# Kernel tuning notes

Hardware: AMD Instinct MI355X
Metric: run time of the kernel (lower is better)

## Reference

```python
import jax, jax.numpy as jnp
import numpy as np

T, B, D_MODEL, H, FFN = 2048, 2, 128, 8, 1024
EPS = 1e-5
NEG = -1e9


def setup_inputs() -> dict:
    key = jax.random.key(0)
    ks = jax.random.split(key, 20)
    d = D_MODEL
    w = lambda k, sh: (jax.random.normal(k, sh, jnp.float32) * 0.02)
    z = lambda n: jnp.zeros((n,), jnp.float32)
    o = lambda n: jnp.ones((n,), jnp.float32)
    return {
        "x": jax.random.normal(ks[0], (T, B, d), jnp.float32),
        "enc": jax.random.normal(ks[1], (T, B, d), jnp.float32),
        "sa_wq": w(ks[2], (d, d)), "sa_bq": z(d),
        "sa_wk": w(ks[3], (d, d)), "sa_bk": z(d),
        "sa_wv": w(ks[4], (d, d)), "sa_bv": z(d),
        "sa_wo": w(ks[5], (d, d)), "sa_bo": z(d),
        "ln1_g": o(d), "ln1_b": z(d),
        "ca_wq": w(ks[6], (d, d)), "ca_bq": z(d),
        "ca_wk": w(ks[7], (d, d)), "ca_bk": z(d),
        "ca_wv": w(ks[8], (d, d)), "ca_bv": z(d),
        "ca_wo": w(ks[9], (d, d)), "ca_bo": z(d),
        "ln2_g": o(d), "ln2_b": z(d),
        "fc1_w": w(ks[10], (d, FFN)), "fc1_b": z(FFN),
        "fc2_w": w(ks[11], (FFN, d)), "fc2_b": z(d),
        "ln3_g": o(d), "ln3_b": z(d),
    }


def _ln(x, g, b):
    m = jnp.mean(x, -1, keepdims=True)
    v = jnp.mean(jnp.square(x - m), -1, keepdims=True)
    return (x - m) * jax.lax.rsqrt(v + EPS) * g + b


def _mha(q_in, kv_in, wq, bq, wk, bk, wv, bv, wo, bo, mask):
    # q_in: [T, B, C]; kv_in: [S, B, C]  (Time x Batch x Channel, as in torch src)
    Tq, Bz, C = q_in.shape
    S = kv_in.shape[0]
    Dh = C // H
    q = (q_in @ wq + bq) * (Dh ** -0.5)
    k = kv_in @ wk + bk
    v = kv_in @ wv + bv
    q = q.reshape(Tq, Bz, H, Dh)
    k = k.reshape(S, Bz, H, Dh)
    v = v.reshape(S, Bz, H, Dh)
    scores = jnp.einsum('tbhd,sbhd->bhts', q, k)  # materialized [B,H,T,S]
    if mask is not None:
        scores = scores + mask  # additive causal mask, broadcast over b,h
    probs = jax.nn.softmax(scores, axis=-1)
    out = jnp.einsum('bhts,sbhd->tbhd', probs, v).reshape(Tq, Bz, C)
    return out @ wo + bo


def reference(x, enc,
              sa_wq, sa_bq, sa_wk, sa_bk, sa_wv, sa_bv, sa_wo, sa_bo,
              ln1_g, ln1_b,
              ca_wq, ca_bq, ca_wk, ca_bk, ca_wv, ca_bv, ca_wo, ca_bo,
              ln2_g, ln2_b,
              fc1_w, fc1_b, fc2_w, fc2_b,
              ln3_g, ln3_b):
    Tq = x.shape[0]
    causal = jnp.where(jnp.tril(jnp.ones((Tq, Tq), bool)), 0.0, NEG).astype(x.dtype)
    # self-attention block (post-norm, dropout=0 in eval)
    res = x
    x = res + _mha(x, x, sa_wq, sa_bq, sa_wk, sa_bk, sa_wv, sa_bv, sa_wo, sa_bo, causal)
    x = _ln(x, ln1_g, ln1_b)
    # cross-attention block
    res = x
    x = res + _mha(x, enc, ca_wq, ca_bq, ca_wk, ca_bk, ca_wv, ca_bv, ca_wo, ca_bo, None)
    x = _ln(x, ln2_g, ln2_b)
    # FFN block (exact erf gelu, matching torch F.gelu default)
    res = x
    h = jax.nn.gelu(x @ fc1_w + fc1_b, approximate=False)
    x = res + (h @ fc2_w + fc2_b)
    x = _ln(x, ln3_g, ln3_b)
    return x
```

## Files before the change

kernel.cpp:

```cpp
#include <hip/hip_runtime.h>
#include <hip/hip_bf16.h>

#define TT 2048
#define BB 2
#define DM 128
#define HH 8
#define DH 16
#define FFN_N 1024
#define ROWS (TT * BB)
#define EPS_LN 1e-5f
#define NC 8
#define SC (TT / NC)
#define NQ32 (TT / 32)
#define NQP (TT / 64)
#define NBH (BB * HH)

typedef __attribute__((ext_vector_type(8))) short bf16x8;
typedef __attribute__((ext_vector_type(4))) short bf16x4v;
typedef __attribute__((ext_vector_type(4))) float f32x4;
typedef __attribute__((ext_vector_type(16))) float f32x16;

__device__ __forceinline__ short f2bf(float x) {
    __hip_bfloat16 h = __float2bfloat16(x);
    union { __hip_bfloat16 hh; short s; } u; u.hh = h; return u.s;
}

__global__ __launch_bounds__(256) void cvt2(
    const float* __restrict__ a, const float* __restrict__ b,
    short* __restrict__ oa, short* __restrict__ ob, int n)
{
    int i = (blockIdx.x * 256 + threadIdx.x) * 4;
    const float* src = a; short* dst = oa;
    if (i >= n) { i -= n; src = b; dst = ob; }
    float4 f = *(const float4*)(src + i);
    bf16x4v o;
    o[0] = f2bf(f.x); o[1] = f2bf(f.y); o[2] = f2bf(f.z); o[3] = f2bf(f.w);
    *(bf16x4v*)(dst + i) = o;
}

__global__ __launch_bounds__(256) void cvt_w_all(
    const float* w0, const float* w1, const float* w2, const float* w3,
    const float* w4, const float* w5, const float* w6, const float* w7,
    const float* w8, const float* w9,
    short* o0, short* o1, short* o2, short* o3,
    short* o4, short* o5, short* o6, short* o7,
    short* o8, short* o9)
{
    const float* srcs[10] = {w0, w1, w2, w3, w4, w5, w6, w7, w8, w9};
    short* dsts[10] = {o0, o1, o2, o3, o4, o5, o6, o7, o8, o9};
    const int bx = blockIdx.x;
    int wi, tile, K, N;
    if (bx < 128)      { wi = bx >> 4; tile = bx & 15;  K = 128;  N = 128;  }
    else if (bx < 256) { wi = 8;       tile = bx - 128; K = 128;  N = 1024; }
    else               { wi = 9;       tile = bx - 256; K = 1024; N = 128;  }
    const float* src = srcs[wi];
    short* dst = dsts[wi];
    const int ntx = N >> 5;
    const int k0 = (tile / ntx) << 5;
    const int n0 = (tile % ntx) << 5;

    __shared__ float sm[32][33];
    const int j = threadIdx.x & 31;
    const int i0 = threadIdx.x >> 5;
    #pragma unroll
    for (int p = 0; p < 4; ++p) {
        const int ii = i0 + p * 8;
        sm[ii][j] = src[(size_t)(k0 + ii) * N + n0 + j];
    }
    __syncthreads();
    #pragma unroll
    for (int p = 0; p < 4; ++p) {
        const int ii = i0 + p * 8;
        dst[(size_t)(n0 + ii) * K + k0 + j] = f2bf(sm[j][ii]);
    }
}

template<int MODE, int GELU>
__global__ __launch_bounds__(256) void gemm_mfma(
    const short* __restrict__ A, const short* __restrict__ Wt,
    const float* __restrict__ bias, void* __restrict__ outp,
    int M, int N, int K, float scale)
{
    const int tid = threadIdx.x;
    const int w = tid >> 6, lane = tid & 63;
    const int wm = w >> 1, wn = w & 1;
    const int g = lane >> 4, qi = lane & 15;
    const int bm = blockIdx.y * 64 + wm * 32;
    const int bn = blockIdx.x * 64 + wn * 32;

    f32x4 acc[2][2];
    #pragma unroll
    for (int a = 0; a < 2; ++a)
        #pragma unroll
        for (int b = 0; b < 2; ++b) acc[a][b] = (f32x4){0.f, 0.f, 0.f, 0.f};

    for (int k0 = 0; k0 < K; k0 += 32) {
        bf16x8 af[2], bf[2];
        #pragma unroll
        for (int fm = 0; fm < 2; ++fm) {
            const short* p = A + (size_t)(bm + fm * 16 + qi) * K + k0 + g * 4;
            bf16x4v lo = *(const bf16x4v*)p;
            bf16x4v hi = *(const bf16x4v*)(p + 16);
            af[fm][0] = lo[0]; af[fm][1] = lo[1]; af[fm][2] = lo[2]; af[fm][3] = lo[3];
            af[fm][4] = hi[0]; af[fm][5] = hi[1]; af[fm][6] = hi[2]; af[fm][7] = hi[3];
        }
        #pragma unroll
        for (int fn = 0; fn < 2; ++fn) {
            const short* p = Wt + (size_t)(bn + fn * 16 + qi) * K + k0 + g * 4;
            bf16x4v lo = *(const bf16x4v*)p;
            bf16x4v hi = *(const bf16x4v*)(p + 16);
            bf[fn][0] = lo[0]; bf[fn][1] = lo[1]; bf[fn][2] = lo[2]; bf[fn][3] = lo[3];
            bf[fn][4] = hi[0]; bf[fn][5] = hi[1]; bf[fn][6] = hi[2]; bf[fn][7] = hi[3];
        }
        #pragma unroll
        for (int fm = 0; fm < 2; ++fm)
            #pragma unroll
            for (int fn = 0; fn < 2; ++fn)
                acc[fm][fn] = __builtin_amdgcn_mfma_f32_16x16x32_bf16(
                    af[fm], bf[fn], acc[fm][fn], 0, 0, 0);
    }

    #pragma unroll
    for (int fm = 0; fm < 2; ++fm)
        #pragma unroll
        for (int fn = 0; fn < 2; ++fn)
            #pragma unroll
            for (int r = 0; r < 4; ++r) {
                const int m = bm + fm * 16 + g * 4 + r;
                const int n = bn + fn * 16 + qi;
                float v = (acc[fm][fn][r] + bias[n]) * scale;
                if (GELU) v = 0.5f * v * (1.f + erff(v * 0.70710678118654752f));
                ((short*)outp)[(size_t)m * N + n] = f2bf(v);
            }
}

__global__ __launch_bounds__(256) void qkv_gemm(
    const short* __restrict__ A0, const short* __restrict__ A1, const short* __restrict__ A2,
    const short* __restrict__ W0, const short* __restrict__ W1, const short* __restrict__ W2,
    const float* __restrict__ B0, const float* __restrict__ B1, const float* __restrict__ B2,
    short* __restrict__ O0, short* __restrict__ O1, short* __restrict__ O2,
    float s0)
{
    const int z = blockIdx.z;
    const short* A = (z == 0) ? A0 : (z == 1) ? A1 : A2;
    const short* Wt = (z == 0) ? W0 : (z == 1) ? W1 : W2;
    const float* bias = (z == 0) ? B0 : (z == 1) ? B1 : B2;
    short* out = (z == 0) ? O0 : (z == 1) ? O1 : O2;
    const float scale = (z == 0) ? s0 : 1.f;
    const int K = DM, N = DM;

    const int tid = threadIdx.x;
    const int w = tid >> 6, lane = tid & 63;
    const int wm = w >> 1, wn = w & 1;
    const int g = lane >> 4, qi = lane & 15;
    const int bm = blockIdx.y * 64 + wm * 32;
    const int bn = blockIdx.x * 64 + wn * 32;

    f32x4 acc[2][2];
    #pragma unroll
    for (int a = 0; a < 2; ++a)
        #pragma unroll
        for (int b = 0; b < 2; ++b) acc[a][b] = (f32x4){0.f, 0.f, 0.f, 0.f};

    for (int k0 = 0; k0 < K; k0 += 32) {
        bf16x8 af[2], bf[2];
        #pragma unroll
        for (int fm = 0; fm < 2; ++fm) {
            const short* p = A + (size_t)(bm + fm * 16 + qi) * K + k0 + g * 4;
            bf16x4v lo = *(const bf16x4v*)p;
            bf16x4v hi = *(const bf16x4v*)(p + 16);
            af[fm][0] = lo[0]; af[fm][1] = lo[1]; af[fm][2] = lo[2]; af[fm][3] = lo[3];
            af[fm][4] = hi[0]; af[fm][5] = hi[1]; af[fm][6] = hi[2]; af[fm][7] = hi[3];
        }
        #pragma unroll
        for (int fn = 0; fn < 2; ++fn) {
            const short* p = Wt + (size_t)(bn + fn * 16 + qi) * K + k0 + g * 4;
            bf16x4v lo = *(const bf16x4v*)p;
            bf16x4v hi = *(const bf16x4v*)(p + 16);
            bf[fn][0] = lo[0]; bf[fn][1] = lo[1]; bf[fn][2] = lo[2]; bf[fn][3] = lo[3];
            bf[fn][4] = hi[0]; bf[fn][5] = hi[1]; bf[fn][6] = hi[2]; bf[fn][7] = hi[3];
        }
        #pragma unroll
        for (int fm = 0; fm < 2; ++fm)
            #pragma unroll
            for (int fn = 0; fn < 2; ++fn)
                acc[fm][fn] = __builtin_amdgcn_mfma_f32_16x16x32_bf16(
                    af[fm], bf[fn], acc[fm][fn], 0, 0, 0);
    }

    #pragma unroll
    for (int fm = 0; fm < 2; ++fm)
        #pragma unroll
        for (int fn = 0; fn < 2; ++fn)
            #pragma unroll
            for (int r = 0; r < 4; ++r) {
                const int m = bm + fm * 16 + g * 4 + r;
                const int n = bn + fn * 16 + qi;
                const float v = (acc[fm][fn][r] + bias[n]) * scale;
                const int t = m >> 1, bz = m & 1, hH = n >> 4, d = n & 15;
                size_t idx;
                if (z < 2) {
                    const int dp = ((d >> 2) & 1) * 8 + (d & 3) + ((d >> 3) & 1) * 4;
                    idx = ((size_t)(bz * HH + hH) * TT + t) * DH + dp;
                } else {
                    const int u = t & 15;
                    const int tp = (t & ~15) | (((u >> 2) & 1) * 8 + (u & 3) + ((u >> 3) & 1) * 4);
                    idx = ((size_t)(bz * HH + hH) * DH + d) * TT + tp;
                }
                out[idx] = f2bf(v);
            }
}

template<int CAUSAL>
__global__ __launch_bounds__(256, 4) void attn_part(
    const short* __restrict__ Qh, const short* __restrict__ Kh,
    const short* __restrict__ Vt, float* __restrict__ pacc,
    float* __restrict__ pml)
{
    const int wv = threadIdx.x >> 6;
    const int lane = threadIdx.x & 63;
    const int tsk = blockIdx.x * 4 + wv;
    const int bh = tsk >> 8;
    const int rr = tsk & 255;
    const int c = rr & (NC - 1);
    const int qp0 = rr >> 3;
    const int qp = (qp0 * 13 + c * 5) & (NQP - 1);
    const int qtA = qp * 64;
    const int qtB = qtA + 32;
    const int start = c * SC;
    const int send = CAUSAL ? min(start + SC, qtB + 32) : (start + SC);
    if (CAUSAL && start >= send) return;

    const int q = lane & 31;
    const int h = lane >> 5;

    const bf16x8 qf1 = *(const bf16x8*)(Qh + ((size_t)bh * TT + qtA + q) * DH + h * 8);
    const bf16x8 qf2 = *(const bf16x8*)(Qh + ((size_t)bh * TT + qtB + q) * DH + h * 8);

    f32x16 acc1, acc2;
    #pragma unroll
    for (int i = 0; i < 16; ++i) { acc1[i] = 0.f; acc2[i] = 0.f; }
    float l1 = 0.f, l2 = 0.f;

    for (int sb = start; sb < send; sb += 32) {
        const bf16x8 kf = *(const bf16x8*)(Kh + ((size_t)bh * TT + sb + q) * DH + h * 8);
        f32x16 z;
        #pragma unroll
        for (int i = 0; i < 16; ++i) z[i] = 0.f;
        f32x16 s1 = __builtin_amdgcn_mfma_f32_32x32x16_bf16(kf, qf1, z, 0, 0, 0);
        f32x16 s2 = __builtin_amdgcn_mfma_f32_32x32x16_bf16(kf, qf2, z, 0, 0, 0);

        if (CAUSAL && (sb + 31 > qtA)) {
            #pragma unroll
            for (int r = 0; r < 16; ++r) {
                const int s_glob = sb + (r & 3) + 8 * (r >> 2) + 4 * h;
                if (s_glob > qtA + q) s1[r] = -1.0e30f;
                if (s_glob > qtB + q) s2[r] = -1.0e30f;
            }
        }

        float c1 = 0.f, c2 = 0.f;
        #pragma unroll
        for (int i = 0; i < 16; ++i) {
            const float p1 = exp2f(s1[i]);
            const float p2 = exp2f(s2[i]);
            s1[i] = p1; s2[i] = p2;
            c1 += p1; c2 += p2;
        }
        l1 += c1; l2 += c2;

        #pragma unroll
        for (int j = 0; j < 2; ++j) {
            bf16x8 pf1, pf2;
            #pragma unroll
            for (int e = 0; e < 8; ++e) { pf1[e] = f2bf(s1[8 * j + e]); pf2[e] = f2bf(s2[8 * j + e]); }
            const bf16x8 vf = *(const bf16x8*)(Vt + ((size_t)bh * DH + q) * TT + sb + 16 * j + h * 8);
            acc1 = __builtin_amdgcn_mfma_f32_32x32x16_bf16(pf1, vf, acc1, 0, 0, 0);
            acc2 = __builtin_amdgcn_mfma_f32_32x32x16_bf16(pf2, vf, acc2, 0, 0, 0);
        }
    }

    l1 += __shfl_xor(l1, 32);
    l2 += __shfl_xor(l2, 32);

    const int qt32A = qp * 2, qt32B = qp * 2 + 1;
    const size_t tA = ((size_t)bh * NQ32 + qt32A) * NC + c;
    const size_t tB = ((size_t)bh * NQ32 + qt32B) * NC + c;
    const int d = q;
    if (d < 16) {
        float* pb1 = pacc + tA * 512 + (size_t)d * 32;
        float* pb2 = pacc + tB * 512 + (size_t)d * 32;
        *(f32x4*)(pb1 + 4 * h)      = (f32x4){acc1[0],  acc1[1],  acc1[2],  acc1[3]};
        *(f32x4*)(pb1 + 8 + 4 * h)  = (f32x4){acc1[4],  acc1[5],  acc1[6],  acc1[7]};
        *(f32x4*)(pb1 + 16 + 4 * h) = (f32x4){acc1[8],  acc1[9],  acc1[10], acc1[11]};
        *(f32x4*)(pb1 + 24 + 4 * h) = (f32x4){acc1[12], acc1[13], acc1[14], acc1[15]};
        *(f32x4*)(pb2 + 4 * h)      = (f32x4){acc2[0],  acc2[1],  acc2[2],  acc2[3]};
        *(f32x4*)(pb2 + 8 + 4 * h)  = (f32x4){acc2[4],  acc2[5],  acc2[6],  acc2[7]};
        *(f32x4*)(pb2 + 16 + 4 * h) = (f32x4){acc2[8],  acc2[9],  acc2[10], acc2[11]};
        *(f32x4*)(pb2 + 24 + 4 * h) = (f32x4){acc2[12], acc2[13], acc2[14], acc2[15]};
    }
    if (h == 0) {
        pml[tA * 32 + q] = l1;
        pml[tB * 32 + q] = l2;
    }
}

__global__ __launch_bounds__(256) void attn_merge(
    const float* __restrict__ pacc, const float* __restrict__ pml,
    short* __restrict__ outb, int causal)
{
    const int wv = threadIdx.x >> 6;
    const int lane = threadIdx.x & 63;
    const int task2 = blockIdx.x * 4 + wv;
    const int qt32 = task2 & (NQ32 - 1);
    const int bh = task2 >> 6;
    const int bz = bh / HH, head = bh % HH;
    const int qt = qt32 * 32;
    const int q = lane & 31, h = lane >> 5;
    const int qp = qt32 >> 1;
    const int nc = causal ? min(NC, (qp * 64 + 64 + SC - 1) / SC) : NC;
    const size_t base = (size_t)task2 * NC;

    float L = 0.f;
    float o[8] = {0.f, 0.f, 0.f, 0.f, 0.f, 0.f, 0.f, 0.f};
    for (int c = 0; c < nc; ++c) {
        L += pml[(base + c) * 32 + q];
        const float* pb = pacc + (base + c) * 512 + (size_t)h * 8 * 32 + q;
        #pragma unroll
        for (int dd = 0; dd < 8; ++dd) o[dd] += pb[dd * 32];
    }

    const float inv = 1.f / L;
    short* op = outb + ((size_t)(qt + q) * BB + bz) * DM + head * DH + h * 8;
    bf16x8 ov;
    #pragma unroll
    for (int dd = 0; dd < 8; ++dd) ov[dd] = f2bf(o[dd] * inv);
    *(bf16x8*)op = ov;
}

template<int KSTEPS>
__global__ __launch_bounds__(256) void lngemm(
    const short* __restrict__ A, const short* __restrict__ Wt,
    const float* __restrict__ bias, const float* __restrict__ resid,
    const float* __restrict__ lg, const float* __restrict__ lb,
    float* __restrict__ outF, short* __restrict__ outB)
{
    const int tid = threadIdx.x;
    const int w = tid >> 6;
    const int lane = tid & 63;
    const int ch = w & 1, kh = w >> 1;
    const int gq = lane >> 4, qi = lane & 15;
    const int m0 = blockIdx.x * 16;
    const int K = KSTEPS * 32;
    const int KH = KSTEPS / 2;

    f32x4 acc[4];
    #pragma unroll
    for (int fn = 0; fn < 4; ++fn) acc[fn] = (f32x4){0.f, 0.f, 0.f, 0.f};

    for (int ks = kh * KH; ks < kh * KH + KH; ++ks) {
        const int k0 = ks * 32;
        bf16x8 af;
        {
            const short* p = A + (size_t)(m0 + qi) * K + k0 + gq * 4;
            bf16x4v lo = *(const bf16x4v*)p;
            bf16x4v hi = *(const bf16x4v*)(p + 16);
            af[0] = lo[0]; af[1] = lo[1]; af[2] = lo[2]; af[3] = lo[3];
            af[4] = hi[0]; af[5] = hi[1]; af[6] = hi[2]; af[7] = hi[3];
        }
        #pragma unroll
        for (int fn = 0; fn < 4; ++fn) {
            const short* p = Wt + (size_t)(ch * 64 + fn * 16 + qi) * K + k0 + gq * 4;
            bf16x4v lo = *(const bf16x4v*)p;
            bf16x4v hi = *(const bf16x4v*)(p + 16);
            bf16x8 bf;
            bf[0] = lo[0]; bf[1] = lo[1]; bf[2] = lo[2]; bf[3] = lo[3];
            bf[4] = hi[0]; bf[5] = hi[1]; bf[6] = hi[2]; bf[7] = hi[3];
            acc[fn] = __builtin_amdgcn_mfma_f32_16x16x32_bf16(af, bf, acc[fn], 0, 0, 0);
        }
    }

    __shared__ float part[16][130];
    __shared__ float smean[2][16], ssq[2][16];

    if (kh == 1) {
        #pragma unroll
        for (int fn = 0; fn < 4; ++fn)
            #pragma unroll
            for (int r = 0; r < 4; ++r)
                part[gq * 4 + r][ch * 64 + fn * 16 + qi] = acc[fn][r];
    }
    __syncthreads();

    float vv[4][4];
    if (kh == 0) {
        #pragma unroll
        for (int fn = 0; fn < 4; ++fn) {
            const int n = ch * 64 + fn * 16 + qi;
            const float bn = bias[n];
            #pragma unroll
            for (int r = 0; r < 4; ++r) {
                const int m = m0 + gq * 4 + r;
                vv[fn][r] = acc[fn][r] + part[gq * 4 + r][n] + bn
                          + resid[(size_t)m * DM + n];
            }
        }
        float ps[4], pq[4];
        #pragma unroll
        for (int r = 0; r < 4; ++r) {
            float s = 0.f, q2 = 0.f;
            #pragma unroll
            for (int fn = 0; fn < 4; ++fn) { s += vv[fn][r]; q2 += vv[fn][r] * vv[fn][r]; }
            #pragma unroll
            for (int off = 1; off < 16; off <<= 1) {
                s += __shfl_xor(s, off);
                q2 += __shfl_xor(q2, off);
            }
            ps[r] = s; pq[r] = q2;
        }
        if (qi == 0) {
            #pragma unroll
            for (int r = 0; r < 4; ++r) {
                smean[ch][gq * 4 + r] = ps[r];
                ssq[ch][gq * 4 + r] = pq[r];
            }
        }
    }
    __syncthreads();

    if (kh == 0) {
        #pragma unroll
        for (int r = 0; r < 4; ++r) {
            const int row = gq * 4 + r;
            const int m = m0 + row;
            const float mean = (smean[0][row] + smean[1][row]) * (1.f / DM);
            const float var = (ssq[0][row] + ssq[1][row]) * (1.f / DM) - mean * mean;
            const float rstd = rsqrtf(var + EPS_LN);
            #pragma unroll
            for (int fn = 0; fn < 4; ++fn) {
                const int n = ch * 64 + fn * 16 + qi;
                const float val = (vv[fn][r] - mean) * rstd * lg[n] + lb[n];
                outF[(size_t)m * DM + n] = val;
                if (outB) outB[(size_t)m * DM + n] = f2bf(val);
            }
        }
    }
}

extern "C" void kernel_launch(void* const* d_in, const int* in_sizes, int n_in,
                              void* d_out, int out_size, void* d_ws, size_t ws_size,
                              hipStream_t stream)
{
    const float* x     = (const float*)d_in[0];
    const float* enc   = (const float*)d_in[1];
    const float* sa_wq = (const float*)d_in[2];
    const float* sa_bq = (const float*)d_in[3];
    const float* sa_wk = (const float*)d_in[4];
    const float* sa_bk = (const float*)d_in[5];
    const float* sa_wv = (const float*)d_in[6];
    const float* sa_bv = (const float*)d_in[7];
    const float* sa_wo = (const float*)d_in[8];
    const float* sa_bo = (const float*)d_in[9];
    const float* ln1_g = (const float*)d_in[10];
    const float* ln1_b = (const float*)d_in[11];
    const float* ca_wq = (const float*)d_in[12];
    const float* ca_bq = (const float*)d_in[13];
    const float* ca_wk = (const float*)d_in[14];
    const float* ca_bk = (const float*)d_in[15];
    const float* ca_wv = (const float*)d_in[16];
    const float* ca_bv = (const float*)d_in[17];
    const float* ca_wo = (const float*)d_in[18];
    const float* ca_bo = (const float*)d_in[19];
    const float* ln2_g = (const float*)d_in[20];
    const float* ln2_b = (const float*)d_in[21];
    const float* fc1_w = (const float*)d_in[22];
    const float* fc1_b = (const float*)d_in[23];
    const float* fc2_w = (const float*)d_in[24];
    const float* fc2_b = (const float*)d_in[25];
    const float* ln3_g = (const float*)d_in[26];
    const float* ln3_b = (const float*)d_in[27];

    float* out = (float*)d_out;
    char* ws = (char*)d_ws;

    const size_t NE = (size_t)ROWS * DM;
    float* b5   = (float*)ws;    ws += NE * 4;
    float* b6   = (float*)ws;    ws += NE * 4;
    float* pacc = (float*)ws;    ws += (size_t)NBH * NQ32 * NC * 512 * 4;
    float* pml  = (float*)ws;    ws += (size_t)NBH * NQ32 * NC * 64 * 4;
    short* xb   = (short*)ws;    ws += NE * 2;
    short* encb = (short*)ws;    ws += NE * 2;
    short* b5b  = (short*)ws;    ws += NE * 2;
    short* b6b  = (short*)ws;    ws += NE * 2;
    short* b3b  = (short*)ws;    ws += NE * 2;
    short* qh   = (short*)ws;    ws += NE * 2;
    short* kh   = (short*)ws;    ws += NE * 2 + 4096;
    short* vt   = (short*)ws;    ws += NE * 2 + 132 * 1024;
    short* hb   = (short*)ws;    ws += (size_t)ROWS * FFN_N * 2;
    short* wt_saq = (short*)ws;  ws += DM * DM * 2;
    short* wt_sak = (short*)ws;  ws += DM * DM * 2;
    short* wt_sav = (short*)ws;  ws += DM * DM * 2;
    short* wt_sao = (short*)ws;  ws += DM * DM * 2;
    short* wt_caq = (short*)ws;  ws += DM * DM * 2;
    short* wt_cak = (short*)ws;  ws += DM * DM * 2;
    short* wt_cav = (short*)ws;  ws += DM * DM * 2;
    short* wt_cao = (short*)ws;  ws += DM * DM * 2;
    short* wt_fc1 = (short*)ws;  ws += DM * FFN_N * 2;
    short* wt_fc2 = (short*)ws;  ws += FFN_N * DM * 2;

    const float qscale = 0.25f * 1.4426950408889634f;
    const dim3 qkvgrid(DM / 64, ROWS / 64, 3);
    const dim3 partgrid(NBH * NQP * NC / 4);
    const dim3 mergegrid(NBH * NQ32 / 4);
    const dim3 lngrid(ROWS / 16);
    const dim3 fc1grid(FFN_N / 64, ROWS / 64);

    hipLaunchKernelGGL(cvt2, dim3(2 * NE / 1024), dim3(256), 0, stream,
                       x, enc, xb, encb, (int)NE);
    hipLaunchKernelGGL(cvt_w_all, dim3(384), dim3(256), 0, stream,
                       sa_wq, sa_wk, sa_wv, sa_wo, ca_wq, ca_wk, ca_wv, ca_wo, fc1_w, fc2_w,
                       wt_saq, wt_sak, wt_sav, wt_sao, wt_caq, wt_cak, wt_cav, wt_cao, wt_fc1, wt_fc2);

    hipLaunchKernelGGL(qkv_gemm, qkvgrid, dim3(256), 0, stream,
                       xb, xb, xb, wt_saq, wt_sak, wt_sav, sa_bq, sa_bk, sa_bv,
                       qh, kh, vt, qscale);
    hipLaunchKernelGGL((attn_part<1>), partgrid, dim3(256), 0, stream, qh, kh, vt, pacc, pml);
    hipLaunchKernelGGL(attn_merge, mergegrid, dim3(256), 0, stream, pacc, pml, b3b, 1);
    hipLaunchKernelGGL((lngemm<4>), lngrid, dim3(256), 0, stream,
                       b3b, wt_sao, sa_bo, x, ln1_g, ln1_b, b5, b5b);

    hipLaunchKernelGGL(qkv_gemm, qkvgrid, dim3(256), 0, stream,
                       b5b, encb, encb, wt_caq, wt_cak, wt_cav, ca_bq, ca_bk, ca_bv,
                       qh, kh, vt, qscale);
    hipLaunchKernelGGL((attn_part<0>), partgrid, dim3(256), 0, stream, qh, kh, vt, pacc, pml);
    hipLaunchKernelGGL(attn_merge, mergegrid, dim3(256), 0, stream, pacc, pml, b3b, 0);
    hipLaunchKernelGGL((lngemm<4>), lngrid, dim3(256), 0, stream,
                       b3b, wt_cao, ca_bo, b5, ln2_g, ln2_b, b6, b6b);

    hipLaunchKernelGGL((gemm_mfma<1,1>), fc1grid, dim3(256), 0, stream,
                       b6b, wt_fc1, fc1_b, hb, ROWS, FFN_N, DM, 1.f);
    hipLaunchKernelGGL((lngemm<32>), lngrid, dim3(256), 0, stream,
                       hb, wt_fc2, fc2_b, b6, ln3_g, ln3_b, out, (short*)nullptr);
}
```

Measured before the change: 145.2 us.

## Fuse input conversion, cross-attn KV projection, merge, and Q projection into neighbours

```diff
diff --git a/kernel.cpp b/kernel.cpp
--- a/kernel.cpp
+++ b/kernel.cpp
@@ -23,19 +23,6 @@
 __device__ __forceinline__ short f2bf(float x) {
     __hip_bfloat16 h = __float2bfloat16(x);
     union { __hip_bfloat16 hh; short s; } u; u.hh = h; return u.s;
-}
-
-__global__ __launch_bounds__(256) void cvt2(
-    const float* __restrict__ a, const float* __restrict__ b,
-    short* __restrict__ oa, short* __restrict__ ob, int n)
-{
-    int i = (blockIdx.x * 256 + threadIdx.x) * 4;
-    const float* src = a; short* dst = oa;
-    if (i >= n) { i -= n; src = b; dst = ob; }
-    float4 f = *(const float4*)(src + i);
-    bf16x4v o;
-    o[0] = f2bf(f.x); o[1] = f2bf(f.y); o[2] = f2bf(f.z); o[3] = f2bf(f.w);
-    *(bf16x4v*)(dst + i) = o;
 }
 
 __global__ __launch_bounds__(256) void cvt_w_all(
@@ -134,22 +121,31 @@
             }
 }
 
-__global__ __launch_bounds__(256) void qkv_gemm(
-    const short* __restrict__ A0, const short* __restrict__ A1, const short* __restrict__ A2,
+__global__ __launch_bounds__(256) void qkv5(
+    const float* __restrict__ x, const float* __restrict__ enc,
     const short* __restrict__ W0, const short* __restrict__ W1, const short* __restrict__ W2,
+    const short* __restrict__ W3, const short* __restrict__ W4,
     const float* __restrict__ B0, const float* __restrict__ B1, const float* __restrict__ B2,
+    const float* __restrict__ B3, const float* __restrict__ B4,
     short* __restrict__ O0, short* __restrict__ O1, short* __restrict__ O2,
-    float s0)
+    short* __restrict__ O3, short* __restrict__ O4,
+    int* __restrict__ ctr1, int* __restrict__ ctr2, float s0)
 {
     const int z = blockIdx.z;
-    const short* A = (z == 0) ? A0 : (z == 1) ? A1 : A2;
-    const short* Wt = (z == 0) ? W0 : (z == 1) ? W1 : W2;
-    const float* bias = (z == 0) ? B0 : (z == 1) ? B1 : B2;
-    short* out = (z == 0) ? O0 : (z == 1) ? O1 : O2;
+    const float* A = (z < 3) ? x : enc;
+    const short* Wt = (z == 0) ? W0 : (z == 1) ? W1 : (z == 2) ? W2 : (z == 3) ? W3 : W4;
+    const float* bias = (z == 0) ? B0 : (z == 1) ? B1 : (z == 2) ? B2 : (z == 3) ? B3 : B4;
+    short* out = (z == 0) ? O0 : (z == 1) ? O1 : (z == 2) ? O2 : (z == 3) ? O3 : O4;
     const float scale = (z == 0) ? s0 : 1.f;
+    const int vmode = (z == 2 || z == 4);
     const int K = DM, N = DM;
 
     const int tid = threadIdx.x;
+    if (z == 0) {
+        const int id = (blockIdx.y * 2 + blockIdx.x) * 256 + tid;
+        if (id < NBH * NQP) { ctr1[id] = 0; ctr2[id] = 0; }
+    }
+
     const int w = tid >> 6, lane = tid & 63;
     const int wm = w >> 1, wn = w & 1;
     const int g = lane >> 4, qi = lane & 15;
@@ -166,11 +162,11 @@
         bf16x8 af[2], bf[2];
         #pragma unroll
         for (int fm = 0; fm < 2; ++fm) {
-            const short* p = A + (size_t)(bm + fm * 16 + qi) * K + k0 + g * 4;
-            bf16x4v lo = *(const bf16x4v*)p;
-            bf16x4v hi = *(const bf16x4v*)(p + 16);
-            af[fm][0] = lo[0]; af[fm][1] = lo[1]; af[fm][2] = lo[2]; af[fm][3] = lo[3];
-            af[fm][4] = hi[0]; af[fm][5] = hi[1]; af[fm][6] = hi[2]; af[fm][7] = hi[3];
+            const float* p = A + (size_t)(bm + fm * 16 + qi) * K + k0 + g * 4;
+            float4 lo = *(const float4*)p;
+            float4 hi = *(const float4*)(p + 16);
+            af[fm][0] = f2bf(lo.x); af[fm][1] = f2bf(lo.y); af[fm][2] = f2bf(lo.z); af[fm][3] = f2bf(lo.w);
+            af[fm][4] = f2bf(hi.x); af[fm][5] = f2bf(hi.y); af[fm][6] = f2bf(hi.z); af[fm][7] = f2bf(hi.w);
         }
         #pragma unroll
         for (int fn = 0; fn < 2; ++fn) {
@@ -199,7 +195,7 @@
                 const float v = (acc[fm][fn][r] + bias[n]) * scale;
                 const int t = m >> 1, bz = m & 1, hH = n >> 4, d = n & 15;
                 size_t idx;
-                if (z < 2) {
+                if (!vmode) {
                     const int dp = ((d >> 2) & 1) * 8 + (d & 3) + ((d >> 3) & 1) * 4;
                     idx = ((size_t)(bz * HH + hH) * TT + t) * DH + dp;
                 } else {
@@ -214,8 +210,8 @@
 template<int CAUSAL>
 __global__ __launch_bounds__(256, 4) void attn_part(
     const short* __restrict__ Qh, const short* __restrict__ Kh,
-    const short* __restrict__ Vt, float* __restrict__ pacc,
-    float* __restrict__ pml)
+    const short* __restrict__ Vt, float* pacc, float* pml,
+    int* ctr, short* __restrict__ outb)
 {
     const int wv = threadIdx.x >> 6;
     const int lane = threadIdx.x & 63;
@@ -283,9 +279,8 @@
     l1 += __shfl_xor(l1, 32);
     l2 += __shfl_xor(l2, 32);
 
-    const int qt32A = qp * 2, qt32B = qp * 2 + 1;
-    const size_t tA = ((size_t)bh * NQ32 + qt32A) * NC + c;
-    const size_t tB = ((size_t)bh * NQ32 + qt32B) * NC + c;
+    const size_t tA = ((size_t)bh * NQ32 + qp * 2) * NC + c;
+    const size_t tB = ((size_t)bh * NQ32 + qp * 2 + 1) * NC + c;
     const int d = q;
     if (d < 16) {
         float* pb1 = pacc + tA * 512 + (size_t)d * 32;
@@ -303,47 +298,44 @@
         pml[tA * 32 + q] = l1;
         pml[tB * 32 + q] = l2;
     }
-}
-
-__global__ __launch_bounds__(256) void attn_merge(
-    const float* __restrict__ pacc, const float* __restrict__ pml,
-    short* __restrict__ outb, int causal)
-{
-    const int wv = threadIdx.x >> 6;
-    const int lane = threadIdx.x & 63;
-    const int task2 = blockIdx.x * 4 + wv;
-    const int qt32 = task2 & (NQ32 - 1);
-    const int bh = task2 >> 6;
+
+    const int ncp = CAUSAL ? min(NC, (qp * 64 + 64 + SC - 1) / SC) : NC;
+    __threadfence();
+    int old = 0;
+    if (lane == 0) old = atomicAdd(&ctr[bh * NQP + qp], 1);
+    old = __shfl(old, 0);
+    if (old != ncp - 1) return;
+    __threadfence();
+
     const int bz = bh / HH, head = bh % HH;
-    const int qt = qt32 * 32;
-    const int q = lane & 31, h = lane >> 5;
-    const int qp = qt32 >> 1;
-    const int nc = causal ? min(NC, (qp * 64 + 64 + SC - 1) / SC) : NC;
-    const size_t base = (size_t)task2 * NC;
-
-    float L = 0.f;
-    float o[8] = {0.f, 0.f, 0.f, 0.f, 0.f, 0.f, 0.f, 0.f};
-    for (int c = 0; c < nc; ++c) {
-        L += pml[(base + c) * 32 + q];
-        const float* pb = pacc + (base + c) * 512 + (size_t)h * 8 * 32 + q;
-        #pragma unroll
-        for (int dd = 0; dd < 8; ++dd) o[dd] += pb[dd * 32];
-    }
-
-    const float inv = 1.f / L;
-    short* op = outb + ((size_t)(qt + q) * BB + bz) * DM + head * DH + h * 8;
-    bf16x8 ov;
-    #pragma unroll
-    for (int dd = 0; dd < 8; ++dd) ov[dd] = f2bf(o[dd] * inv);
-    *(bf16x8*)op = ov;
-}
-
-template<int KSTEPS>
+    #pragma unroll
+    for (int tile = 0; tile < 2; ++tile) {
+        const size_t base = ((size_t)bh * NQ32 + qp * 2 + tile) * NC;
+        float L = 0.f;
+        float o[8] = {0.f, 0.f, 0.f, 0.f, 0.f, 0.f, 0.f, 0.f};
+        for (int cc = 0; cc < ncp; ++cc) {
+            L += pml[(base + cc) * 32 + q];
+            const float* pb = pacc + (base + cc) * 512 + (size_t)h * 8 * 32 + q;
+            #pragma unroll
+            for (int dd = 0; dd < 8; ++dd) o[dd] += pb[dd * 32];
+        }
+        const float inv = 1.f / L;
+        short* op = outb + ((size_t)(qp * 64 + tile * 32 + q) * BB + bz) * DM + head * DH + h * 8;
+        bf16x8 ov;
+        #pragma unroll
+        for (int dd = 0; dd < 8; ++dd) ov[dd] = f2bf(o[dd] * inv);
+        *(bf16x8*)op = ov;
+    }
+}
+
+template<int KSTEPS, int QPROJ>
 __global__ __launch_bounds__(256) void lngemm(
     const short* __restrict__ A, const short* __restrict__ Wt,
     const float* __restrict__ bias, const float* __restrict__ resid,
     const float* __restrict__ lg, const float* __restrict__ lb,
-    float* __restrict__ outF, short* __restrict__ outB)
+    float* __restrict__ outF, short* __restrict__ outB,
+    const short* __restrict__ Wq, const float* __restrict__ bq,
+    short* __restrict__ Oq, float qs)
 {
     const int tid = threadIdx.x;
     const int w = tid >> 6;
@@ -354,6 +346,10 @@
     const int K = KSTEPS * 32;
     const int KH = KSTEPS / 2;
 
+    __shared__ float part[16][130];
+    __shared__ float smean[2][16], ssq[2][16];
+    __shared__ short Alds[16][136];
+
     f32x4 acc[4];
     #pragma unroll
     for (int fn = 0; fn < 4; ++fn) acc[fn] = (f32x4){0.f, 0.f, 0.f, 0.f};
@@ -380,9 +376,6 @@
         }
     }
 
-    __shared__ float part[16][130];
-    __shared__ float smean[2][16], ssq[2][16];
-
     if (kh == 1) {
         #pragma unroll
         for (int fn = 0; fn < 4; ++fn)
@@ -441,9 +434,48 @@
                 const int n = ch * 64 + fn * 16 + qi;
                 const float val = (vv[fn][r] - mean) * rstd * lg[n] + lb[n];
                 outF[(size_t)m * DM + n] = val;
-                if (outB) outB[(size_t)m * DM + n] = f2bf(val);
-            }
-        }
+                const short vb = f2bf(val);
+                if (outB) outB[(size_t)m * DM + n] = vb;
+                if (QPROJ) Alds[row][n] = vb;
+            }
+        }
+    }
+
+    if (QPROJ) {
+        __syncthreads();
+        f32x4 qacc[2];
+        qacc[0] = (f32x4){0.f, 0.f, 0.f, 0.f};
+        qacc[1] = (f32x4){0.f, 0.f, 0.f, 0.f};
+        for (int ks = 0; ks < 4; ++ks) {
+            const int k0 = ks * 32;
+            bf16x8 af;
+            {
+                const short* p = &Alds[qi][k0 + gq * 4];
+                af[0] = p[0]; af[1] = p[1]; af[2] = p[2]; af[3] = p[3];
+                af[4] = p[16]; af[5] = p[17]; af[6] = p[18]; af[7] = p[19];
+            }
+            #pragma unroll
+            for (int fn = 0; fn < 2; ++fn) {
+                const short* p = Wq + (size_t)(w * 32 + fn * 16 + qi) * DM + k0 + gq * 4;
+                bf16x4v lo = *(const bf16x4v*)p;
+                bf16x4v hi = *(const bf16x4v*)(p + 16);
+                bf16x8 bf;
+                bf[0] = lo[0]; bf[1] = lo[1]; bf[2] = lo[2]; bf[3] = lo[3];
+                bf[4] = hi[0]; bf[5] = hi[1]; bf[6] = hi[2]; bf[7] = hi[3];
+                qacc[fn] = __builtin_amdgcn_mfma_f32_16x16x32_bf16(af, bf, qacc[fn], 0, 0, 0);
+            }
+        }
+        #pragma unroll
+        for (int fn = 0; fn < 2; ++fn)
+            #pragma unroll
+            for (int r = 0; r < 4; ++r) {
+                const int m = m0 + gq * 4 + r;
+                const int n = w * 32 + fn * 16 + qi;
+                const float v = (qacc[fn][r] + bq[n]) * qs;
+                const int t = m >> 1, bz = m & 1, hH = n >> 4, d = n & 15;
+                const int dp = ((d >> 2) & 1) * 8 + (d & 3) + ((d >> 3) & 1) * 4;
+                Oq[((size_t)(bz * HH + hH) * TT + t) * DH + dp] = f2bf(v);
+            }
     }
 }
 
@@ -488,15 +520,16 @@
     float* b6   = (float*)ws;    ws += NE * 4;
     float* pacc = (float*)ws;    ws += (size_t)NBH * NQ32 * NC * 512 * 4;
     float* pml  = (float*)ws;    ws += (size_t)NBH * NQ32 * NC * 64 * 4;
-    short* xb   = (short*)ws;    ws += NE * 2;
-    short* encb = (short*)ws;    ws += NE * 2;
-    short* b5b  = (short*)ws;    ws += NE * 2;
     short* b6b  = (short*)ws;    ws += NE * 2;
     short* b3b  = (short*)ws;    ws += NE * 2;
     short* qh   = (short*)ws;    ws += NE * 2;
     short* kh   = (short*)ws;    ws += NE * 2 + 4096;
     short* vt   = (short*)ws;    ws += NE * 2 + 132 * 1024;
+    short* kh2  = (short*)ws;    ws += NE * 2 + 4096;
+    short* vt2  = (short*)ws;    ws += NE * 2 + 132 * 1024;
     short* hb   = (short*)ws;    ws += (size_t)ROWS * FFN_N * 2;
+    int*   ctr1 = (int*)ws;      ws += 2048;
+    int*   ctr2 = (int*)ws;      ws += 2048;
     short* wt_saq = (short*)ws;  ws += DM * DM * 2;
     short* wt_sak = (short*)ws;  ws += DM * DM * 2;
     short* wt_sav = (short*)ws;  ws += DM * DM * 2;
@@ -509,36 +542,31 @@
     short* wt_fc2 = (short*)ws;  ws += FFN_N * DM * 2;
 
     const float qscale = 0.25f * 1.4426950408889634f;
-    const dim3 qkvgrid(DM / 64, ROWS / 64, 3);
+    const dim3 qkvgrid(DM / 64, ROWS / 64, 5);
     const dim3 partgrid(NBH * NQP * NC / 4);
-    const dim3 mergegrid(NBH * NQ32 / 4);
     const dim3 lngrid(ROWS / 16);
     const dim3 fc1grid(FFN_N / 64, ROWS / 64);
 
-    hipLaunchKernelGGL(cvt2, dim3(2 * NE / 1024), dim3(256), 0, stream,
-                       x, enc, xb, encb, (int)NE);
     hipLaunchKernelGGL(cvt_w_all, dim3(384), dim3(256), 0, stream,
                        sa_wq, sa_wk, sa_wv, sa_wo, ca_wq, ca_wk, ca_wv, ca_wo, fc1_w, fc2_w,
                        wt_saq, wt_sak, wt_sav, wt_sao, wt_caq, wt_cak, wt_cav, wt_cao, wt_fc1, wt_fc2);
-
-    hipLaunchKernelGGL(qkv_gemm, qkvgrid, dim3(256), 0, stream,
-                       xb, xb, xb, wt_saq, wt_sak, wt_sav, sa_bq, sa_bk, sa_bv,
-                       qh, kh, vt, qscale);
-    hipLaunchKernelGGL((attn_part<1>), partgrid, dim3(256), 0, stream, qh, kh, vt, pacc, pml);
-    hipLaunchKernelGGL(attn_merge, mergegrid, dim3(256), 0, stream, pacc, pml, b3b, 1);
-    hipLaunchKernelGGL((lngemm<4>), lngrid, dim3(256), 0, stream,
-                       b3b, wt_sao, sa_bo, x, ln1_g, ln1_b, b5, b5b);
-
-    hipLaunchKernelGGL(qkv_gemm, qkvgrid, dim3(256), 0, stream,
-                       b5b, encb, encb, wt_caq, wt_cak, wt_cav, ca_bq, ca_bk, ca_bv,
-                       qh, kh, vt, qscale);
-    hipLaunchKernelGGL((attn_part<0>), partgrid, dim3(256), 0, stream, qh, kh, vt, pacc, pml);
-    hipLaunchKernelGGL(attn_merge, mergegrid, dim3(256), 0, stream, pacc, pml, b3b, 0);
-    hipLaunchKernelGGL((lngemm<4>), lngrid, dim3(256), 0, stream,
-                       b3b, wt_cao, ca_bo, b5, ln2_g, ln2_b, b6, b6b);
-
-    hipLaunchKernelGGL((gemm_mfma<1,1>), fc1grid, dim3(256), 0, stream,
+    hipLaunchKernelGGL(qkv5, qkvgrid, dim3(256), 0, stream,
+                       x, enc, wt_saq, wt_sak, wt_sav, wt_cak, wt_cav,
+                       sa_bq, sa_bk, sa_bv, ca_bk, ca_bv,
+                       qh, kh, vt, kh2, vt2, ctr1, ctr2, qscale);
+    hipLaunchKernelGGL((attn_part<1>), partgrid, dim3(256), 0, stream,
+                       qh, kh, vt, pacc, pml, ctr1, b3b);
+    hipLaunchKernelGGL((lngemm<4, 1>), lngrid, dim3(256), 0, stream,
+                       b3b, wt_sao, sa_bo, x, ln1_g, ln1_b, b5, (short*)nullptr,
+                       wt_caq, ca_bq, qh, qscale);
+    hipLaunchKernelGGL((attn_part<0>), partgrid, dim3(256), 0, stream,
+                       qh, kh2, vt2, pacc, pml, ctr2, b3b);
+    hipLaunchKernelGGL((lngemm<4, 0>), lngrid, dim3(256), 0, stream,
+                       b3b, wt_cao, ca_bo, b5, ln2_g, ln2_b, b6, b6b,
+                       (const short*)nullptr, (const float*)nullptr, (short*)nullptr, 1.f);
+    hipLaunchKernelGGL((gemm_mfma<1, 1>), fc1grid, dim3(256), 0, stream,
                        b6b, wt_fc1, fc1_b, hb, ROWS, FFN_N, DM, 1.f);
-    hipLaunchKernelGGL((lngemm<32>), lngrid, dim3(256), 0, stream,
-                       hb, wt_fc2, fc2_b, b6, ln3_g, ln3_b, out, (short*)nullptr);
-}
+    hipLaunchKernelGGL((lngemm<32, 0>), lngrid, dim3(256), 0, stream,
+                       hb, wt_fc2, fc2_b, b6, ln3_g, ln3_b, out, (short*)nullptr,
+                       (const short*)nullptr, (const float*)nullptr, (short*)nullptr, 1.f);
+}
```

After: 503.4 us. 247% more time.
